# Kernel optimization log

Hardware: AMD Instinct MI355X
Metric: run time of the kernel (lower is better)

The kernel has to match this reference:

```python
import jax, jax.numpy as jnp
import numpy as np
import math

B, L, D = 4, 4096, 512
P, V = 128, 8  # n_phases, value_dim
PI = math.pi

def _lin(x, w, b):
    return x @ w + b

def _gelu(x):
    return jax.nn.gelu(x, approximate=False)  # torch default exact GELU

def setup_inputs() -> dict:
    key = jax.random.key(0)
    ks = iter(jax.random.split(key, 32))
    def rn(shape, scale=0.02):
        return (jax.random.normal(next(ks), shape, dtype=jnp.float32) * scale)
    inp = {
        'x': jax.random.normal(next(ks), (B, L, D), dtype=jnp.float32),
        'pos_phases': jax.random.normal(next(ks), (L, D), dtype=jnp.float32) * PI,
        'magnitude_scale': jnp.float32(5.0),
        'w_v': rn((D, D)), 'b_v': jnp.zeros((D,), jnp.float32),
        'w_o': rn((D, D)), 'b_o': jnp.zeros((D,), jnp.float32),
        'w_m': rn((D, D)), 'b_m': jnp.zeros((D,), jnp.float32),
        'w_q': rn((D, D)), 'b_q': jnp.zeros((D,), jnp.float32),
        'w_ke': rn((D, P)), 'b_ke': jnp.zeros((P,), jnp.float32),
        'w_ve': rn((D, V)), 'b_ve': jnp.zeros((V,), jnp.float32),
        'w_s1': rn((2 * D, D)), 'b_s1': jnp.zeros((D,), jnp.float32),
        'w_s2': rn((D, P)), 'b_s2': jnp.zeros((P,), jnp.float32),
        'w_g': rn((D, 1)), 'b_g': jnp.zeros((1,), jnp.float32),
        'w_kv': rn((V, D)), 'b_kv': jnp.zeros((D,), jnp.float32),
        'ln_g': jnp.ones((2 * D,), jnp.float32), 'ln_b': jnp.zeros((2 * D,), jnp.float32),
        'w_t1': rn((2 * D, 2 * D)), 'b_t1': jnp.zeros((2 * D,), jnp.float32),
        'w_t2': rn((2 * D, D)), 'b_t2': jnp.zeros((D,), jnp.float32),
    }
    return inp

def _forward(x, pos_phases, magnitude_scale, w_v, b_v, w_o, b_o, w_m, b_m,
             w_q, b_q, w_ke, b_ke, w_ve, b_ve, w_s1, b_s1, w_s2, b_s2,
             w_g, b_g, w_kv, b_kv, ln_g, ln_b, w_t1, b_t1, w_t2, b_t2):
    b, l, d = x.shape
    phi = pos_phases[:l]                               # [L,D]
    cos_phi, sin_phi = jnp.cos(phi), jnp.sin(phi)
    # --- positional phasor memory ---
    v1 = _lin(x, w_v, b_v)                             # [B,L,D]
    magnitude = jax.nn.sigmoid(_lin(x, w_m, b_m)) * jnp.abs(magnitude_scale)
    weighted_v1 = magnitude * v1
    mem1_cos = jnp.cumsum(weighted_v1 * cos_phi, axis=1)
    mem1_sin = jnp.cumsum(weighted_v1 * sin_phi, axis=1)
    sqrt_mag = jnp.sqrt(jnp.cumsum(magnitude, axis=1) + 1e-8)
    mem1_cos = mem1_cos / sqrt_mag
    mem1_sin = mem1_sin / sqrt_mag
    phi_query = phi + _lin(x, w_q, b_q)
    pos_ret = (mem1_cos * jnp.cos(phi_query) + mem1_sin * jnp.sin(phi_query)) / math.sqrt(d)
    pos_out = _lin(pos_ret, w_o, b_o)                  # [B,L,D]
    # --- key-value phasor memory ---
    query_phase = jnp.tanh(_lin(x, w_ke, b_ke)) * PI   # [B,L,P]
    values = _lin(x, w_ve, b_ve)                       # [B,L,V]
    store_gate = jax.nn.sigmoid(_lin(x, w_g, b_g))     # [B,L,1]
    positions = jnp.arange(1, l + 1, dtype=x.dtype)[None, :, None]
    context_avg = jnp.cumsum(x, axis=1) / positions
    sk = _lin(_gelu(_lin(jnp.concatenate([x, context_avg], axis=-1), w_s1, b_s1)), w_s2, b_s2)
    storage_phase = jnp.tanh(sk) * PI                  # [B,L,P]
    gv = values * store_gate                           # [B,L,V]
    kv_bound_cos = jnp.cos(storage_phase)[..., None] * gv[:, :, None, :]  # [B,L,P,V]
    kv_bound_sin = jnp.sin(storage_phase)[..., None] * gv[:, :, None, :]
    kv_mem_cos = jnp.cumsum(kv_bound_cos, axis=1)
    kv_mem_sin = jnp.cumsum(kv_bound_sin, axis=1)
    gate_cumsum = jnp.clip(jnp.cumsum(store_gate, axis=1), 1.0, None)     # [B,L,1]
    inv = 1.0 / jnp.sqrt(gate_cumsum)[..., None]
    kv_mem_cos = kv_mem_cos * inv
    kv_mem_sin = kv_mem_sin * inv
    kv_retrieved = (jnp.cos(query_phase)[..., None] * kv_mem_cos
                    + jnp.sin(query_phase)[..., None] * kv_mem_sin).sum(axis=2) / math.sqrt(P)
    kv_out = _lin(kv_retrieved, w_kv, b_kv)            # [B,L,D]
    # --- output projection (dropout = eval/identity) ---
    combined = jnp.concatenate([pos_out, kv_out], axis=-1)  # [B,L,2D]
    mu = combined.mean(axis=-1, keepdims=True)
    var = combined.var(axis=-1, keepdims=True)
    ln = (combined - mu) / jnp.sqrt(var + 1e-5) * ln_g + ln_b
    return x + _lin(_gelu(_lin(ln, w_t1, b_t1)), w_t2, b_t2)

def reference(x, pos_phases, magnitude_scale, w_v, b_v, w_o, b_o, w_m, b_m,
              w_q, b_q, w_ke, b_ke, w_ve, b_ve, w_s1, b_s1, w_s2, b_s2,
              w_g, b_g, w_kv, b_kv, ln_g, ln_b, w_t1, b_t1, w_t2, b_t2):
    return _forward(x, pos_phases, magnitude_scale, w_v, b_v, w_o, b_o, w_m, b_m,
                    w_q, b_q, w_ke, b_ke, w_ve, b_ve, w_s1, b_s1, w_s2, b_s2,
                    w_g, b_g, w_kv, b_kv, ln_g, ln_b, w_t1, b_t1, w_t2, b_t2)
```

## Files before the change

kernel.cpp:

```cpp
#include <hip/hip_runtime.h>
#include <math.h>

#define NTOK 16384
#define LSEQ 4096
#define BATCH 4
#define DDIM 512
#define PDIM 128
#define VDIM 8
#define PI_F 3.14159265358979323846f

#define NC2 64
#define CL2 64
#define NC3 128
#define CL3 32

typedef __attribute__((ext_vector_type(8))) short bfrag8;
typedef __attribute__((ext_vector_type(4))) float facc4;

__device__ __forceinline__ float sigmoid_(float v) { return 1.0f / (1.0f + expf(-v)); }
__device__ __forceinline__ float gelu_(float v) { return 0.5f * v * (1.0f + erff(v * 0.70710678118654752f)); }

__device__ __forceinline__ unsigned short f2bf(float f) {
    unsigned int u = __builtin_bit_cast(unsigned int, f);
    u += 0x7fffu + ((u >> 16) & 1u);
    return (unsigned short)(u >> 16);
}
__device__ __forceinline__ float bf2f(unsigned short h) {
    return __builtin_bit_cast(float, ((unsigned int)h) << 16);
}
__device__ __forceinline__ float bflo(unsigned int w) { return __builtin_bit_cast(float, w << 16); }
__device__ __forceinline__ float bfhi(unsigned int w) { return __builtin_bit_cast(float, w & 0xffff0000u); }

__device__ __forceinline__ void async16(const unsigned short* g, unsigned short* l) {
    __builtin_amdgcn_global_load_lds(
        (const __attribute__((address_space(1))) unsigned int*)g,
        (__attribute__((address_space(3))) unsigned int*)l, 16, 0, 0);
}

__global__ __launch_bounds__(256) void gemm_bf16(
    const unsigned short* __restrict__ A, int ldA,
    const unsigned short* __restrict__ Wt,
    const float* __restrict__ bias, int K,
    float* __restrict__ Cf, unsigned short* __restrict__ Cb, int ldC, int colOff,
    const float* __restrict__ res, int ldRes,
    int act)
{
    __shared__ unsigned short Asm[128 * 32];
    __shared__ unsigned short Bsm[128 * 32];
    const int tid = threadIdx.x;
    const int lane = tid & 63;
    const int wv = tid >> 6;
    const int wm = wv & 1, wn = wv >> 1;
    const int quad = lane >> 4, cc = lane & 15;
    const int row0 = blockIdx.y << 7;
    const int col0 = blockIdx.x << 7;

    facc4 acc[4][4];
#pragma unroll
    for (int i = 0; i < 4; ++i)
#pragma unroll
        for (int j = 0; j < 4; ++j) acc[i][j] = (facc4){0.f, 0.f, 0.f, 0.f};

    const int rquad = tid >> 2;
    const int kq = tid & 3;

    for (int k0 = 0; k0 < K; k0 += 32) {
        __syncthreads();
        {
            const unsigned short* ga0 = A + (size_t)(row0 + rquad) * ldA + k0 + kq * 8;
            const unsigned short* ga1 = A + (size_t)(row0 + 64 + rquad) * ldA + k0 + kq * 8;
            async16(ga0, &Asm[tid * 8]);
            async16(ga1, &Asm[(256 + tid) * 8]);
            const unsigned short* gb0 = Wt + (size_t)(col0 + rquad) * K + k0 + kq * 8;
            const unsigned short* gb1 = Wt + (size_t)(col0 + 64 + rquad) * K + k0 + kq * 8;
            async16(gb0, &Bsm[tid * 8]);
            async16(gb1, &Bsm[(256 + tid) * 8]);
        }
        __syncthreads();
        bfrag8 afr[4], bfr[4];
#pragma unroll
        for (int mt = 0; mt < 4; ++mt)
            afr[mt] = *(const bfrag8*)&Asm[(wm * 64 + mt * 16 + cc) * 32 + quad * 8];
#pragma unroll
        for (int nt = 0; nt < 4; ++nt)
            bfr[nt] = *(const bfrag8*)&Bsm[(wn * 64 + nt * 16 + cc) * 32 + quad * 8];
#pragma unroll
        for (int mt = 0; mt < 4; ++mt)
#pragma unroll
            for (int nt = 0; nt < 4; ++nt)
                acc[mt][nt] = __builtin_amdgcn_mfma_f32_16x16x32_bf16(
                    afr[mt], bfr[nt], acc[mt][nt], 0, 0, 0);
    }

#pragma unroll
    for (int nt = 0; nt < 4; ++nt) {
        int col = col0 + wn * 64 + nt * 16 + cc;
        float bvv = bias[col];
#pragma unroll
        for (int mt = 0; mt < 4; ++mt) {
            int rowb = row0 + wm * 64 + mt * 16 + quad * 4;
#pragma unroll
            for (int r = 0; r < 4; ++r) {
                float v = acc[mt][nt][r] + bvv;
                if (act == 1) v = gelu_(v);
                size_t row = (size_t)(rowb + r);
                if (res) v += res[row * ldRes + col];
                size_t idx = row * ldC + colOff + col;
                if (Cf) Cf[idx] = v;
                else    Cb[idx] = f2bf(v);
            }
        }
    }
}

__global__ __launch_bounds__(256) void k_wcvt(const float* __restrict__ W, int K, int N,
                                              unsigned short* __restrict__ Wt)
{
    __shared__ float t[32][33];
    int bx = blockIdx.x, by = blockIdx.y;
    int tid = threadIdx.x;
    int tx = tid & 31, ty = tid >> 5;
#pragma unroll
    for (int r = 0; r < 4; ++r) {
        int k = by * 32 + ty + r * 8;
        t[ty + r * 8][tx] = W[(size_t)k * N + bx * 32 + tx];
    }
    __syncthreads();
#pragma unroll
    for (int r = 0; r < 4; ++r) {
        int n = bx * 32 + ty + r * 8;
        Wt[(size_t)n * K + by * 32 + tx] = f2bf(t[tx][ty + r * 8]);
    }
}

__global__ void k_xcvt(const float* __restrict__ x, unsigned short* __restrict__ xcat)
{
    int g = blockIdx.x * 256 + threadIdx.x;
    int c = g & 511, r = g >> 9;
    xcat[(size_t)r * 1024 + c] = f2bf(x[g]);
}

__global__ void k_phi(const float* __restrict__ pp, float* __restrict__ cphi,
                      float* __restrict__ sphi, int n)
{
    int i = blockIdx.x * 256 + threadIdx.x;
    if (i < n) {
        float s, c;
        sincosf(pp[i], &s, &c);
        cphi[i] = c;
        sphi[i] = s;
    }
}

__global__ __launch_bounds__(256) void k_glin(const float* __restrict__ x,
                                              const float* __restrict__ wg,
                                              const float* __restrict__ bg,
                                              float* __restrict__ glin)
{
    int wid = threadIdx.x >> 6, lane = threadIdx.x & 63;
    int row = blockIdx.x * 4 + wid;
    const float4* xr = (const float4*)(x + (size_t)row * DDIM);
    const float4* w4 = (const float4*)wg;
    float4 a0 = xr[lane], a1 = xr[lane + 64];
    float4 w0 = w4[lane], w1 = w4[lane + 64];
    float p = a0.x * w0.x + a0.y * w0.y + a0.z * w0.z + a0.w * w0.w
            + a1.x * w1.x + a1.y * w1.y + a1.z * w1.z + a1.w * w1.w;
    for (int d = 32; d >= 1; d >>= 1) p += __shfl_down(p, d, 64);
    if (lane == 0) glin[row] = p + bg[0];
}

__global__ __launch_bounds__(256) void k_values(const float* __restrict__ x,
                                                const float* __restrict__ wve,
                                                const float* __restrict__ bve,
                                                const float* __restrict__ glin,
                                                float* __restrict__ gv)
{
    int g = blockIdx.x * 256 + threadIdx.x;
    int m = g & 7, r = g >> 3;
    const float4* xr = (const float4*)(x + (size_t)r * DDIM);
    float acc = bve[m];
    for (int kq = 0; kq < 128; ++kq) {
        float4 a = xr[kq];
        int k = kq * 4;
        acc += a.x * wve[k * 8 + m] + a.y * wve[(k + 1) * 8 + m]
             + a.z * wve[(k + 2) * 8 + m] + a.w * wve[(k + 3) * 8 + m];
    }
    gv[g] = acc * sigmoid_(glin[r]);
}

__global__ __launch_bounds__(256) void k_scan1a(
    const unsigned short* __restrict__ v1, const unsigned short* __restrict__ mlin,
    const float* __restrict__ x,
    const float* __restrict__ cphi, const float* __restrict__ sphi,
    const float* __restrict__ msp, float* __restrict__ sum2)
{
    int g = blockIdx.x * 256 + threadIdx.x;
    int d = g & 511;
    int rest = g >> 9;
    int chunk = rest & (NC2 - 1);
    int b = rest >> 6;
    float msabs = fabsf(msp[0]);
    size_t base = ((size_t)b * LSEQ + chunk * CL2) * DDIM + d;
    size_t pbase = ((size_t)chunk * CL2) * DDIM + d;
    float ac = 0.f, as = 0.f, am = 0.f, ax = 0.f;
    for (int i = 0; i < CL2; ++i) {
        float ml = bf2f(mlin[base]), vv = bf2f(v1[base]), xv = x[base];
        float cp = cphi[pbase], sp = sphi[pbase];
        float mag = msabs * sigmoid_(ml);
        float wv = mag * vv;
        ac += wv * cp; as += wv * sp; am += mag; ax += xv;
        base += DDIM; pbase += DDIM;
    }
    int col = (b * DDIM + d) * NC2 + chunk;
    sum2[0 * 131072 + col] = ac;
    sum2[1 * 131072 + col] = as;
    sum2[2 * 131072 + col] = am;
    sum2[3 * 131072 + col] = ax;
}

__global__ __launch_bounds__(256) void k_scan1b(float* __restrict__ sum2)
{
    int g = blockIdx.x * 256 + threadIdx.x;
    float* p = sum2 + (size_t)g * NC2;
    float run = 0.f;
    for (int i = 0; i < NC2; ++i) { float t = p[i]; p[i] = run; run += t; }
}

__global__ __launch_bounds__(256) void k_scan1c(
    const unsigned short* __restrict__ v1, const unsigned short* __restrict__ mlin,
    const unsigned short* __restrict__ qlin, const float* __restrict__ x,
    const float* __restrict__ cphi, const float* __restrict__ sphi,
    const float* __restrict__ msp, const float* __restrict__ sum2,
    unsigned short* __restrict__ pret, unsigned short* __restrict__ xcat)
{
    int g = blockIdx.x * 256 + threadIdx.x;
    int d = g & 511;
    int rest = g >> 9;
    int chunk = rest & (NC2 - 1);
    int b = rest >> 6;
    float msabs = fabsf(msp[0]);
    int col = (b * DDIM + d) * NC2 + chunk;
    float ac = sum2[col];
    float as = sum2[131072 + col];
    float am = sum2[2 * 131072 + col];
    float ax = sum2[3 * 131072 + col];
    size_t base = ((size_t)b * LSEQ + chunk * CL2) * DDIM + d;
    size_t pbase = ((size_t)chunk * CL2) * DDIM + d;
    int l = chunk * CL2;
    const float rsd = 0.04419417382415922f;
    for (int i = 0; i < CL2; ++i, ++l) {
        float ml = bf2f(mlin[base]), vv = bf2f(v1[base]), xv = x[base];
        float q = bf2f(qlin[base]);
        float cp = cphi[pbase], sp = sphi[pbase];
        float mag = msabs * sigmoid_(ml);
        float wv = mag * vv;
        ac += wv * cp; as += wv * sp; am += mag; ax += xv;
        float inv = rsqrtf(am + 1e-8f);
        float mc = ac * inv, msn = as * inv;
        float cq, sq;
        sincosf(q, &sq, &cq);
        float cpq = cp * cq - sp * sq;
        float spq = sp * cq + cp * sq;
        pret[base] = f2bf((mc * cpq + msn * spq) * rsd);
        size_t row = (size_t)b * LSEQ + l;
        xcat[row * 1024 + 512 + d] = f2bf(ax / (float)(l + 1));
        base += DDIM; pbase += DDIM;
    }
}

__global__ void k_phases(const float* __restrict__ sk, const unsigned short* __restrict__ ke,
                         unsigned short* __restrict__ csp, unsigned short* __restrict__ ssp,
                         unsigned short* __restrict__ cqp, unsigned short* __restrict__ sqp, int n)
{
    int g = blockIdx.x * 256 + threadIdx.x;
    if (g < n) {
        float s, c;
        float spv = tanhf(sk[g]) * PI_F;
        sincosf(spv, &s, &c);
        csp[g] = f2bf(c); ssp[g] = f2bf(s);
        float qpv = tanhf(bf2f(ke[g])) * PI_F;
        sincosf(qpv, &s, &c);
        cqp[g] = f2bf(c); sqp[g] = f2bf(s);
    }
}

__global__ __launch_bounds__(1024) void k_gatescan(const float* __restrict__ glin,
                                                   float* __restrict__ gcum)
{
    __shared__ float s[1024];
    int b = blockIdx.x, tid = threadIdx.x;
    const float* gp = glin + (size_t)b * LSEQ + tid * 4;
    float e0 = sigmoid_(gp[0]);
    float e1 = sigmoid_(gp[1]);
    float e2 = sigmoid_(gp[2]);
    float e3 = sigmoid_(gp[3]);
    float l0 = e0, l1 = l0 + e1, l2 = l1 + e2, l3 = l2 + e3;
    s[tid] = l3;
    __syncthreads();
    for (int off = 1; off < 1024; off <<= 1) {
        float t = (tid >= off) ? s[tid - off] : 0.0f;
        __syncthreads();
        s[tid] += t;
        __syncthreads();
    }
    float excl = s[tid] - l3;
    float* out = gcum + (size_t)b * LSEQ + tid * 4;
    out[0] = excl + l0; out[1] = excl + l1; out[2] = excl + l2; out[3] = excl + l3;
}

__device__ __forceinline__ size_t kv_sum_idx(int b, int p, int v) {
    return ((((size_t)b * PDIM + p) * VDIM + v) * 2) * NC3;
}

__global__ __launch_bounds__(256) void k_kv1(const unsigned short* __restrict__ csp,
                                             const unsigned short* __restrict__ ssp,
                                             const float* __restrict__ gv,
                                             float* __restrict__ sum3)
{
    int blk = blockIdx.x;
    int chunk = blk & (NC3 - 1), b = blk >> 7;
    int tid = threadIdx.x;
    int w = tid >> 6, lane = tid & 63;
    int v = 2 * w + (lane & 1);
    int pq = lane >> 1;
    float sc[4] = {0, 0, 0, 0}, ss[4] = {0, 0, 0, 0};
    const uint2* c2p = (const uint2*)csp;
    const uint2* s2p = (const uint2*)ssp;
    int t = b * LSEQ + chunk * CL3;
    for (int i = 0; i < CL3; ++i, ++t) {
        uint2 cu = c2p[(size_t)t * 32 + pq];
        uint2 su = s2p[(size_t)t * 32 + pq];
        float g = gv[(size_t)t * VDIM + v];
        sc[0] += bflo(cu.x) * g; sc[1] += bfhi(cu.x) * g;
        sc[2] += bflo(cu.y) * g; sc[3] += bfhi(cu.y) * g;
        ss[0] += bflo(su.x) * g; ss[1] += bfhi(su.x) * g;
        ss[2] += bflo(su.y) * g; ss[3] += bfhi(su.y) * g;
    }
#pragma unroll
    for (int j = 0; j < 4; ++j) {
        size_t base = kv_sum_idx(b, pq * 4 + j, v) + chunk;
        sum3[base] = sc[j];
        sum3[base + NC3] = ss[j];
    }
}

__global__ __launch_bounds__(256) void k_kv2(float* __restrict__ sum3)
{
    int g = blockIdx.x * 256 + threadIdx.x;
    float* p = sum3 + (size_t)g * NC3;
    float run = 0.f;
    for (int i = 0; i < NC3; ++i) { float t = p[i]; p[i] = run; run += t; }
}

__global__ __launch_bounds__(256) void k_kv3(const unsigned short* __restrict__ csp,
                                             const unsigned short* __restrict__ ssp,
                                             const unsigned short* __restrict__ cqp,
                                             const unsigned short* __restrict__ sqp,
                                             const float* __restrict__ gv,
                                             const float* __restrict__ gcum,
                                             const float* __restrict__ sum3,
                                             float* __restrict__ kvr)
{
    int blk = blockIdx.x;
    int chunk = blk & (NC3 - 1), b = blk >> 7;
    int tid = threadIdx.x;
    int w = tid >> 6, lane = tid & 63;
    int v = 2 * w + (lane & 1);
    int pq = lane >> 1;
    float sc[4], ss[4];
#pragma unroll
    for (int j = 0; j < 4; ++j) {
        size_t base = kv_sum_idx(b, pq * 4 + j, v) + chunk;
        sc[j] = sum3[base];
        ss[j] = sum3[base + NC3];
    }
    const uint2* c2p = (const uint2*)csp;
    const uint2* s2p = (const uint2*)ssp;
    const uint2* cq2p = (const uint2*)cqp;
    const uint2* sq2p = (const uint2*)sqp;
    const float rsp = 0.08838834764831845f;
    int t = b * LSEQ + chunk * CL3;
    for (int i = 0; i < CL3; ++i, ++t) {
        uint2 cu = c2p[(size_t)t * 32 + pq];
        uint2 su = s2p[(size_t)t * 32 + pq];
        float g = gv[(size_t)t * VDIM + v];
        sc[0] += bflo(cu.x) * g; sc[1] += bfhi(cu.x) * g;
        sc[2] += bflo(cu.y) * g; sc[3] += bfhi(cu.y) * g;
        ss[0] += bflo(su.x) * g; ss[1] += bfhi(su.x) * g;
        ss[2] += bflo(su.y) * g; ss[3] += bfhi(su.y) * g;
        uint2 qcu = cq2p[(size_t)t * 32 + pq];
        uint2 qsu = sq2p[(size_t)t * 32 + pq];
        float part = bflo(qcu.x) * sc[0] + bfhi(qcu.x) * sc[1]
                   + bflo(qcu.y) * sc[2] + bfhi(qcu.y) * sc[3]
                   + bflo(qsu.x) * ss[0] + bfhi(qsu.x) * ss[1]
                   + bflo(qsu.y) * ss[2] + bfhi(qsu.y) * ss[3];
        part += __shfl_down(part, 32, 64);
        part += __shfl_down(part, 16, 64);
        part += __shfl_down(part, 8, 64);
        part += __shfl_down(part, 4, 64);
        part += __shfl_down(part, 2, 64);
        if (lane < 2) {
            float gc = gcum[t];
            float scale = rsqrtf(fmaxf(gc, 1.0f)) * rsp;
            kvr[(size_t)t * VDIM + v] = part * scale;
        }
    }
}

__global__ __launch_bounds__(256) void k_kvout(const float* __restrict__ kvr,
                                               const float* __restrict__ wkv,
                                               const float* __restrict__ bkv,
                                               unsigned short* __restrict__ comb)
{
    int g = blockIdx.x * 256 + threadIdx.x;
    int c = g & 511, r = g >> 9;
    const float* kr = kvr + (size_t)r * VDIM;
    float acc = bkv[c];
#pragma unroll
    for (int k = 0; k < 8; ++k) acc += kr[k] * wkv[k * DDIM + c];
    comb[(size_t)r * 1024 + 512 + c] = f2bf(acc);
}

__global__ __launch_bounds__(256) void k_ln(unsigned short* __restrict__ comb,
                                            const float* __restrict__ gam,
                                            const float* __restrict__ bet)
{
    int wid = threadIdx.x >> 6, lane = threadIdx.x & 63;
    int row = blockIdx.x * 4 + wid;
    unsigned int* rp = (unsigned int*)(comb + (size_t)row * 1024);
    uint4 u0 = *(uint4*)&rp[lane * 8];
    uint4 u1 = *(uint4*)&rp[lane * 8 + 4];
    unsigned int uu[8] = {u0.x, u0.y, u0.z, u0.w, u1.x, u1.y, u1.z, u1.w};
    float v[16];
    float s = 0.f, s2 = 0.f;
#pragma unroll
    for (int j = 0; j < 8; ++j) {
        v[2 * j] = bflo(uu[j]);
        v[2 * j + 1] = bfhi(uu[j]);
        s += v[2 * j] + v[2 * j + 1];
        s2 += v[2 * j] * v[2 * j] + v[2 * j + 1] * v[2 * j + 1];
    }
    for (int m = 32; m >= 1; m >>= 1) {
        s += __shfl_xor(s, m, 64);
        s2 += __shfl_xor(s2, m, 64);
    }
    float mu = s * (1.0f / 1024.0f);
    float var = s2 * (1.0f / 1024.0f) - mu * mu;
    float inv = rsqrtf(var + 1e-5f);
    int c0 = lane * 16;
    unsigned int ou[8];
#pragma unroll
    for (int j = 0; j < 8; ++j) {
        float g0 = gam[c0 + 2 * j], g1 = gam[c0 + 2 * j + 1];
        float b0 = bet[c0 + 2 * j], b1 = bet[c0 + 2 * j + 1];
        float o0 = (v[2 * j] - mu) * inv * g0 + b0;
        float o1 = (v[2 * j + 1] - mu) * inv * g1 + b1;
        ou[j] = (unsigned int)f2bf(o0) | ((unsigned int)f2bf(o1) << 16);
    }
    *(uint4*)&rp[lane * 8] = make_uint4(ou[0], ou[1], ou[2], ou[3]);
    *(uint4*)&rp[lane * 8 + 4] = make_uint4(ou[4], ou[5], ou[6], ou[7]);
}

extern "C" void kernel_launch(void* const* d_in, const int* in_sizes, int n_in,
                              void* d_out, int out_size, void* d_ws, size_t ws_size,
                              hipStream_t stream)
{
    const float* x    = (const float*)d_in[0];
    const float* pp   = (const float*)d_in[1];
    const float* msp  = (const float*)d_in[2];
    const float* w_v  = (const float*)d_in[3];
    const float* b_v  = (const float*)d_in[4];
    const float* w_o  = (const float*)d_in[5];
    const float* b_o  = (const float*)d_in[6];
    const float* w_m  = (const float*)d_in[7];
    const float* b_m  = (const float*)d_in[8];
    const float* w_q  = (const float*)d_in[9];
    const float* b_q  = (const float*)d_in[10];
    const float* w_ke = (const float*)d_in[11];
    const float* b_ke = (const float*)d_in[12];
    const float* w_ve = (const float*)d_in[13];
    const float* b_ve = (const float*)d_in[14];
    const float* w_s1 = (const float*)d_in[15];
    const float* b_s1 = (const float*)d_in[16];
    const float* w_s2 = (const float*)d_in[17];
    const float* b_s2 = (const float*)d_in[18];
    const float* w_g  = (const float*)d_in[19];
    const float* b_g  = (const float*)d_in[20];
    const float* w_kv = (const float*)d_in[21];
    const float* b_kv = (const float*)d_in[22];
    const float* ln_g = (const float*)d_in[23];
    const float* ln_b = (const float*)d_in[24];
    const float* w_t1 = (const float*)d_in[25];
    const float* b_t1 = (const float*)d_in[26];
    const float* w_t2 = (const float*)d_in[27];
    const float* b_t2 = (const float*)d_in[28];
    float* out = (float*)d_out;
    float* ws = (float*)d_ws;
    (void)ws_size; (void)n_in; (void)in_sizes; (void)out_size;

    unsigned short* V1bf   = (unsigned short*)(ws);
    unsigned short* MLINbf = (unsigned short*)(ws + 4194304);
    float*          SKf    = ws + 4194304;
    unsigned short* QLINbf = (unsigned short*)(ws + 8388608);
    unsigned short* CSP    = (unsigned short*)(ws + 8388608);
    unsigned short* SSP    = CSP + 2097152;
    unsigned short* CQP    = CSP + 2 * 2097152;
    unsigned short* SQP    = CSP + 3 * 2097152;
    unsigned short* KEbf   = (unsigned short*)(ws + 12582912);
    float* GVb   = ws + 13631488;
    float* GLINb = ws + 13762560;
    float* GCUMb = ws + 13778944;
    float* SUM2b = ws + 13795328;
    float* SUM3b = ws + 14319616;
    float* KVRb  = ws + 15368192;
    float* CPHIb = ws + 15499264;
    float* SPHIb = ws + 17596416;
    unsigned short* HSbf   = (unsigned short*)(ws + 15499264);
    unsigned short* PRETbf = (unsigned short*)(ws + 19693568);
    unsigned short* XCAT   = (unsigned short*)(ws + 23887872);
    unsigned short* COMBbf = XCAT;
    unsigned short* HTbf   = (unsigned short*)(ws);
    unsigned short* WT     = (unsigned short*)(ws + 32276480);
    unsigned short* wv_t  = WT;
    unsigned short* wm_t  = WT + 262144;
    unsigned short* wq_t  = WT + 524288;
    unsigned short* wo_t  = WT + 786432;
    unsigned short* wke_t = WT + 1048576;
    unsigned short* ws1_t = WT + 1114112;
    unsigned short* ws2_t = WT + 1638400;
    unsigned short* wt1_t = WT + 1703936;
    unsigned short* wt2_t = WT + 2752512;

    k_phi<<<8192, 256, 0, stream>>>(pp, CPHIb, SPHIb, 2097152);
    k_xcvt<<<32768, 256, 0, stream>>>(x, XCAT);
    k_wcvt<<<dim3(16, 16), 256, 0, stream>>>(w_v, 512, 512, wv_t);
    k_wcvt<<<dim3(16, 16), 256, 0, stream>>>(w_m, 512, 512, wm_t);
    k_wcvt<<<dim3(16, 16), 256, 0, stream>>>(w_q, 512, 512, wq_t);
    k_wcvt<<<dim3(16, 16), 256, 0, stream>>>(w_o, 512, 512, wo_t);
    k_wcvt<<<dim3(4, 16), 256, 0, stream>>>(w_ke, 512, 128, wke_t);
    k_wcvt<<<dim3(16, 32), 256, 0, stream>>>(w_s1, 1024, 512, ws1_t);
    k_wcvt<<<dim3(4, 16), 256, 0, stream>>>(w_s2, 512, 128, ws2_t);
    k_wcvt<<<dim3(32, 32), 256, 0, stream>>>(w_t1, 1024, 1024, wt1_t);
    k_wcvt<<<dim3(16, 32), 256, 0, stream>>>(w_t2, 1024, 512, wt2_t);

    gemm_bf16<<<dim3(4, 128), 256, 0, stream>>>(XCAT, 1024, wv_t, b_v, 512, nullptr, V1bf, 512, 0, nullptr, 0, 0);
    gemm_bf16<<<dim3(4, 128), 256, 0, stream>>>(XCAT, 1024, wm_t, b_m, 512, nullptr, MLINbf, 512, 0, nullptr, 0, 0);
    gemm_bf16<<<dim3(4, 128), 256, 0, stream>>>(XCAT, 1024, wq_t, b_q, 512, nullptr, QLINbf, 512, 0, nullptr, 0, 0);
    gemm_bf16<<<dim3(1, 128), 256, 0, stream>>>(XCAT, 1024, wke_t, b_ke, 512, nullptr, KEbf, 128, 0, nullptr, 0, 0);
    k_glin<<<4096, 256, 0, stream>>>(x, w_g, b_g, GLINb);
    k_values<<<512, 256, 0, stream>>>(x, w_ve, b_ve, GLINb, GVb);

    k_scan1a<<<512, 256, 0, stream>>>(V1bf, MLINbf, x, CPHIb, SPHIb, msp, SUM2b);
    k_scan1b<<<32, 256, 0, stream>>>(SUM2b);
    k_scan1c<<<512, 256, 0, stream>>>(V1bf, MLINbf, QLINbf, x, CPHIb, SPHIb, msp, SUM2b, PRETbf, XCAT);

    gemm_bf16<<<dim3(4, 128), 256, 0, stream>>>(XCAT, 1024, ws1_t, b_s1, 1024, nullptr, HSbf, 512, 0, nullptr, 0, 1);
    gemm_bf16<<<dim3(1, 128), 256, 0, stream>>>(HSbf, 512, ws2_t, b_s2, 512, SKf, nullptr, 128, 0, nullptr, 0, 0);

    k_phases<<<8192, 256, 0, stream>>>(SKf, KEbf, CSP, SSP, CQP, SQP, 2097152);
    k_gatescan<<<4, 1024, 0, stream>>>(GLINb, GCUMb);

    k_kv1<<<512, 256, 0, stream>>>(CSP, SSP, GVb, SUM3b);
    k_kv2<<<32, 256, 0, stream>>>(SUM3b);
    k_kv3<<<512, 256, 0, stream>>>(CSP, SSP, CQP, SQP, GVb, GCUMb, SUM3b, KVRb);

    gemm_bf16<<<dim3(4, 128), 256, 0, stream>>>(PRETbf, 512, wo_t, b_o, 512, nullptr, COMBbf, 1024, 0, nullptr, 0, 0);
    k_kvout<<<32768, 256, 0, stream>>>(KVRb, w_kv, b_kv, COMBbf);
    k_ln<<<4096, 256, 0, stream>>>(COMBbf, ln_g, ln_b);
    gemm_bf16<<<dim3(8, 128), 256, 0, stream>>>(COMBbf, 1024, wt1_t, b_t1, 1024, nullptr, HTbf, 1024, 0, nullptr, 0, 1);
    gemm_bf16<<<dim3(4, 128), 256, 0, stream>>>(HTbf, 1024, wt2_t, b_t2, 1024, out, nullptr, 512, 0, x, 512, 0);
}
```

Baseline: 665.8 us.

## Double-buffer GEMM LDS tiles and fuse V/M/Q projections into one GEMM

The bf16 GEMM now keeps two LDS buffers and prefetches the next K-slice with async global-to-LDS loads while MFMAs run on the current one, with one barrier per iteration instead of two. The three 512x512 projections (v, m, q) are merged into a single GEMM with a 1536-wide output row, relying on the three transposed weights sitting next to each other in the weight buffer and on a packed bias vector. The scan kernels read v, m and q from the interleaved buffer. This cuts launch count and barrier stalls, at the cost of doubling GEMM shared memory and relying on workspace layout assumptions.

```diff
diff --git a/kernel.cpp b/kernel.cpp
--- a/kernel.cpp
+++ b/kernel.cpp
@@ -14,6 +14,8 @@
 #define NC3 128
 #define CL3 32
 
+#define VMQ_S 1536
+
 typedef __attribute__((ext_vector_type(8))) short bfrag8;
 typedef __attribute__((ext_vector_type(4))) float facc4;
 
@@ -45,8 +47,8 @@
     const float* __restrict__ res, int ldRes,
     int act)
 {
-    __shared__ unsigned short Asm[128 * 32];
-    __shared__ unsigned short Bsm[128 * 32];
+    __shared__ unsigned short Asm[2][128 * 32];
+    __shared__ unsigned short Bsm[2][128 * 32];
     const int tid = threadIdx.x;
     const int lane = tid & 63;
     const int wv = tid >> 6;
@@ -64,32 +66,42 @@
     const int rquad = tid >> 2;
     const int kq = tid & 3;
 
-    for (int k0 = 0; k0 < K; k0 += 32) {
-        __syncthreads();
-        {
-            const unsigned short* ga0 = A + (size_t)(row0 + rquad) * ldA + k0 + kq * 8;
-            const unsigned short* ga1 = A + (size_t)(row0 + 64 + rquad) * ldA + k0 + kq * 8;
-            async16(ga0, &Asm[tid * 8]);
-            async16(ga1, &Asm[(256 + tid) * 8]);
-            const unsigned short* gb0 = Wt + (size_t)(col0 + rquad) * K + k0 + kq * 8;
-            const unsigned short* gb1 = Wt + (size_t)(col0 + 64 + rquad) * K + k0 + kq * 8;
-            async16(gb0, &Bsm[tid * 8]);
-            async16(gb1, &Bsm[(256 + tid) * 8]);
+    const unsigned short* ga0 = A + (size_t)(row0 + rquad) * ldA + kq * 8;
+    const unsigned short* ga1 = ga0 + (size_t)64 * ldA;
+    const unsigned short* gb0 = Wt + (size_t)(col0 + rquad) * K + kq * 8;
+    const unsigned short* gb1 = gb0 + (size_t)64 * K;
+
+    async16(ga0, &Asm[0][tid * 8]);
+    async16(ga1, &Asm[0][(256 + tid) * 8]);
+    async16(gb0, &Bsm[0][tid * 8]);
+    async16(gb1, &Bsm[0][(256 + tid) * 8]);
+    __syncthreads();
+
+    const int nk = K >> 5;
+    int cur = 0;
+    for (int t = 0; t < nk; ++t) {
+        if (t + 1 < nk) {
+            const int off = (t + 1) << 5;
+            async16(ga0 + off, &Asm[cur ^ 1][tid * 8]);
+            async16(ga1 + off, &Asm[cur ^ 1][(256 + tid) * 8]);
+            async16(gb0 + off, &Bsm[cur ^ 1][tid * 8]);
+            async16(gb1 + off, &Bsm[cur ^ 1][(256 + tid) * 8]);
         }
-        __syncthreads();
         bfrag8 afr[4], bfr[4];
 #pragma unroll
         for (int mt = 0; mt < 4; ++mt)
-            afr[mt] = *(const bfrag8*)&Asm[(wm * 64 + mt * 16 + cc) * 32 + quad * 8];
+            afr[mt] = *(const bfrag8*)&Asm[cur][(wm * 64 + mt * 16 + cc) * 32 + quad * 8];
 #pragma unroll
         for (int nt = 0; nt < 4; ++nt)
-            bfr[nt] = *(const bfrag8*)&Bsm[(wn * 64 + nt * 16 + cc) * 32 + quad * 8];
+            bfr[nt] = *(const bfrag8*)&Bsm[cur][(wn * 64 + nt * 16 + cc) * 32 + quad * 8];
 #pragma unroll
         for (int mt = 0; mt < 4; ++mt)
 #pragma unroll
             for (int nt = 0; nt < 4; ++nt)
                 acc[mt][nt] = __builtin_amdgcn_mfma_f32_16x16x32_bf16(
                     afr[mt], bfr[nt], acc[mt][nt], 0, 0, 0);
+        __syncthreads();
+        cur ^= 1;
     }
 
 #pragma unroll
@@ -140,6 +152,15 @@
     xcat[(size_t)r * 1024 + c] = f2bf(x[g]);
 }
 
+__global__ void k_bpack(const float* __restrict__ b0, const float* __restrict__ b1,
+                        const float* __restrict__ b2, float* __restrict__ dst)
+{
+    int i = blockIdx.x * 256 + threadIdx.x;
+    if (i < 512) dst[i] = b0[i];
+    else if (i < 1024) dst[i] = b1[i - 512];
+    else if (i < 1536) dst[i] = b2[i - 1024];
+}
+
 __global__ void k_phi(const float* __restrict__ pp, float* __restrict__ cphi,
                       float* __restrict__ sphi, int n)
 {
@@ -189,8 +210,7 @@
 }
 
 __global__ __launch_bounds__(256) void k_scan1a(
-    const unsigned short* __restrict__ v1, const unsigned short* __restrict__ mlin,
-    const float* __restrict__ x,
+    const unsigned short* __restrict__ vmq, const float* __restrict__ x,
     const float* __restrict__ cphi, const float* __restrict__ sphi,
     const float* __restrict__ msp, float* __restrict__ sum2)
 {
@@ -200,16 +220,20 @@
     int chunk = rest & (NC2 - 1);
     int b = rest >> 6;
     float msabs = fabsf(msp[0]);
-    size_t base = ((size_t)b * LSEQ + chunk * CL2) * DDIM + d;
+    size_t row = (size_t)b * LSEQ + chunk * CL2;
+    const unsigned short* vp = vmq + row * VMQ_S + d;
+    const float* xp = x + row * DDIM + d;
     size_t pbase = ((size_t)chunk * CL2) * DDIM + d;
     float ac = 0.f, as = 0.f, am = 0.f, ax = 0.f;
     for (int i = 0; i < CL2; ++i) {
-        float ml = bf2f(mlin[base]), vv = bf2f(v1[base]), xv = x[base];
+        float vv = bf2f(vp[0]);
+        float ml = bf2f(vp[512]);
+        float xv = xp[0];
         float cp = cphi[pbase], sp = sphi[pbase];
         float mag = msabs * sigmoid_(ml);
         float wv = mag * vv;
         ac += wv * cp; as += wv * sp; am += mag; ax += xv;
-        base += DDIM; pbase += DDIM;
+        vp += VMQ_S; xp += DDIM; pbase += DDIM;
     }
     int col = (b * DDIM + d) * NC2 + chunk;
     sum2[0 * 131072 + col] = ac;
@@ -227,8 +251,7 @@
 }
 
 __global__ __launch_bounds__(256) void k_scan1c(
-    const unsigned short* __restrict__ v1, const unsigned short* __restrict__ mlin,
-    const unsigned short* __restrict__ qlin, const float* __restrict__ x,
+    const unsigned short* __restrict__ vmq, const float* __restrict__ x,
     const float* __restrict__ cphi, const float* __restrict__ sphi,
     const float* __restrict__ msp, const float* __restrict__ sum2,
     unsigned short* __restrict__ pret, unsigned short* __restrict__ xcat)
@@ -244,13 +267,17 @@
     float as = sum2[131072 + col];
     float am = sum2[2 * 131072 + col];
     float ax = sum2[3 * 131072 + col];
-    size_t base = ((size_t)b * LSEQ + chunk * CL2) * DDIM + d;
+    size_t row = (size_t)b * LSEQ + chunk * CL2;
+    const unsigned short* vp = vmq + row * VMQ_S + d;
+    size_t base = row * DDIM + d;
     size_t pbase = ((size_t)chunk * CL2) * DDIM + d;
     int l = chunk * CL2;
     const float rsd = 0.04419417382415922f;
     for (int i = 0; i < CL2; ++i, ++l) {
-        float ml = bf2f(mlin[base]), vv = bf2f(v1[base]), xv = x[base];
-        float q = bf2f(qlin[base]);
+        float vv = bf2f(vp[0]);
+        float ml = bf2f(vp[512]);
+        float q = bf2f(vp[1024]);
+        float xv = x[base];
         float cp = cphi[pbase], sp = sphi[pbase];
         float mag = msabs * sigmoid_(ml);
         float wv = mag * vv;
@@ -262,9 +289,9 @@
         float cpq = cp * cq - sp * sq;
         float spq = sp * cq + cp * sq;
         pret[base] = f2bf((mc * cpq + msn * spq) * rsd);
-        size_t row = (size_t)b * LSEQ + l;
-        xcat[row * 1024 + 512 + d] = f2bf(ax / (float)(l + 1));
-        base += DDIM; pbase += DDIM;
+        size_t orow = (size_t)b * LSEQ + l;
+        xcat[orow * 1024 + 512 + d] = f2bf(ax / (float)(l + 1));
+        vp += VMQ_S; base += DDIM; pbase += DDIM;
     }
 }
 
@@ -498,10 +525,8 @@
     float* ws = (float*)d_ws;
     (void)ws_size; (void)n_in; (void)in_sizes; (void)out_size;
 
-    unsigned short* V1bf   = (unsigned short*)(ws);
-    unsigned short* MLINbf = (unsigned short*)(ws + 4194304);
+    unsigned short* VMQ    = (unsigned short*)(ws);
     float*          SKf    = ws + 4194304;
-    unsigned short* QLINbf = (unsigned short*)(ws + 8388608);
     unsigned short* CSP    = (unsigned short*)(ws + 8388608);
     unsigned short* SSP    = CSP + 2097152;
     unsigned short* CQP    = CSP + 2 * 2097152;
@@ -511,6 +536,7 @@
     float* GLINb = ws + 13762560;
     float* GCUMb = ws + 13778944;
     float* SUM2b = ws + 13795328;
+    float* CBIAS = SUM2b;
     float* SUM3b = ws + 14319616;
     float* KVRb  = ws + 15368192;
     float* CPHIb = ws + 15499264;
@@ -542,17 +568,16 @@
     k_wcvt<<<dim3(4, 16), 256, 0, stream>>>(w_s2, 512, 128, ws2_t);
     k_wcvt<<<dim3(32, 32), 256, 0, stream>>>(w_t1, 1024, 1024, wt1_t);
     k_wcvt<<<dim3(16, 32), 256, 0, stream>>>(w_t2, 1024, 512, wt2_t);
-
-    gemm_bf16<<<dim3(4, 128), 256, 0, stream>>>(XCAT, 1024, wv_t, b_v, 512, nullptr, V1bf, 512, 0, nullptr, 0, 0);
-    gemm_bf16<<<dim3(4, 128), 256, 0, stream>>>(XCAT, 1024, wm_t, b_m, 512, nullptr, MLINbf, 512, 0, nullptr, 0, 0);
-    gemm_bf16<<<dim3(4, 128), 256, 0, stream>>>(XCAT, 1024, wq_t, b_q, 512, nullptr, QLINbf, 512, 0, nullptr, 0, 0);
+    k_bpack<<<6, 256, 0, stream>>>(b_v, b_m, b_q, CBIAS);
+
+    gemm_bf16<<<dim3(12, 128), 256, 0, stream>>>(XCAT, 1024, wv_t, CBIAS, 512, nullptr, VMQ, VMQ_S, 0, nullptr, 0, 0);
     gemm_bf16<<<dim3(1, 128), 256, 0, stream>>>(XCAT, 1024, wke_t, b_ke, 512, nullptr, KEbf, 128, 0, nullptr, 0, 0);
     k_glin<<<4096, 256, 0, stream>>>(x, w_g, b_g, GLINb);
     k_values<<<512, 256, 0, stream>>>(x, w_ve, b_ve, GLINb, GVb);
 
-    k_scan1a<<<512, 256, 0, stream>>>(V1bf, MLINbf, x, CPHIb, SPHIb, msp, SUM2b);
+    k_scan1a<<<512, 256, 0, stream>>>(VMQ, x, CPHIb, SPHIb, msp, SUM2b);
     k_scan1b<<<32, 256, 0, stream>>>(SUM2b);
-    k_scan1c<<<512, 256, 0, stream>>>(V1bf, MLINbf, QLINbf, x, CPHIb, SPHIb, msp, SUM2b, PRETbf, XCAT);
+    k_scan1c<<<512, 256, 0, stream>>>(VMQ, x, CPHIb, SPHIb, msp, SUM2b, PRETbf, XCAT);
 
     gemm_bf16<<<dim3(4, 128), 256, 0, stream>>>(XCAT, 1024, ws1_t, b_s1, 1024, nullptr, HSbf, 512, 0, nullptr, 0, 1);
     gemm_bf16<<<dim3(1, 128), 256, 0, stream>>>(HSbf, 512, ws2_t, b_s2, 512, SKf, nullptr, 128, 0, nullptr, 0, 0);
```

Measured after the change: 648.3 us. 1.03x faster.
